# Performance work log

Hardware: AMD Instinct MI355X
Metric: run time of the kernel (lower is better)

Reference implementation:

```python
import jax, jax.numpy as jnp
import numpy as np
from jax import lax

EMB_DIM = 16
NUM_EMB = 32
DN = ('NCDHW', 'OIDHW', 'NCDHW')


def conv3d(x, w, b, stride, pad):
    y = lax.conv_general_dilated(x, w, window_strides=(stride,) * 3,
                                 padding=[(pad, pad)] * 3, dimension_numbers=DN)
    return y + b[None, :, None, None, None]


def deconv3d(x, w, b, stride, pad):
    # PyTorch ConvTranspose3d: weight (Cin,Cout,k,k,k); equivalent to conv with
    # spatially flipped, channel-transposed kernel, lhs_dilation=stride, pad=k-1-p.
    k = w.shape[-1]
    wf = jnp.flip(w, axis=(2, 3, 4)).transpose(1, 0, 2, 3, 4)  # (Cout,Cin,k,k,k)
    y = lax.conv_general_dilated(x, wf, window_strides=(1, 1, 1),
                                 padding=[(k - 1 - pad, k - 1 - pad)] * 3,
                                 lhs_dilation=(stride,) * 3, dimension_numbers=DN)
    return y + b[None, :, None, None, None]


def setup_inputs() -> dict:
    key = jax.random.key(0)
    ks = jax.random.split(key, 16)
    x = jax.random.normal(ks[0], (16, 3, 16, 128, 128), dtype=jnp.float32)
    s = 0.05
    # encoder params
    enc_w1 = jax.random.normal(ks[1], (4, 3, 4, 4, 4), jnp.float32) * s
    enc_b1 = jnp.zeros((4,), jnp.float32)
    enc_w2 = jax.random.normal(ks[2], (8, 4, 4, 4, 4), jnp.float32) * s
    enc_b2 = jnp.zeros((8,), jnp.float32)
    enc_w4 = jax.random.normal(ks[3], (EMB_DIM, 8, 3, 3, 3), jnp.float32) * s
    enc_b4 = jnp.zeros((EMB_DIM,), jnp.float32)
    # decoder params (ConvTranspose3d layout: (Cin, Cout, k, k, k))
    dec_w1 = jax.random.normal(ks[4], (EMB_DIM, 8, 4, 4, 4), jnp.float32) * s
    dec_b1 = jnp.zeros((8,), jnp.float32)
    dec_w3 = jax.random.normal(ks[5], (8, 4, 4, 4, 4), jnp.float32) * s
    dec_b3 = jnp.zeros((4,), jnp.float32)
    dec_w4 = jax.random.normal(ks[6], (4, 3, 3, 3, 3), jnp.float32) * s
    dec_b4 = jnp.zeros((3,), jnp.float32)
    # codebook buffers: normalize(randn)*0.1, rows 0/1 forced
    e = jax.random.normal(ks[7], (NUM_EMB, EMB_DIM), jnp.float32)
    e = e / jnp.linalg.norm(e, axis=1, keepdims=True) * 0.1
    embedding = e.at[0].set(0.0).at[1].set(6.0)
    cluster_size = jnp.ones((NUM_EMB,), jnp.float32)
    return dict(x=x, epoch=60,
                enc_w1=enc_w1, enc_b1=enc_b1, enc_w2=enc_w2, enc_b2=enc_b2,
                enc_w4=enc_w4, enc_b4=enc_b4,
                dec_w1=dec_w1, dec_b1=dec_b1, dec_w3=dec_w3, dec_b3=dec_b3,
                dec_w4=dec_w4, dec_b4=dec_b4,
                embedding=embedding, cluster_size=cluster_size)


def reference(x, epoch, enc_w1, enc_b1, enc_w2, enc_b2, enc_w4, enc_b4,
              dec_w1, dec_b1, dec_w3, dec_b3, dec_w4, dec_b4,
              embedding, cluster_size):
    # ---- Encoder ----
    h = jax.nn.relu(conv3d(x, enc_w1, enc_b1, 2, 1))
    h = jax.nn.relu(conv3d(h, enc_w2, enc_b2, 2, 1))
    z = jnp.clip(conv3d(h, enc_w4, enc_b4, 1, 1), 0.0, 6.0)  # relu(relu6(.))
    B, C, Dd, Hh, Ww = z.shape

    # ---- VQ-EMA forward (epoch >= 50 branch) ----
    emb = embedding.at[0].set(0.0).at[1].set(6.0)
    flat = z.transpose(0, 2, 3, 4, 1).reshape(-1, C)  # (N, D)
    # squared euclidean distances; argmin matches cdist argmin
    d2 = (jnp.sum(flat * flat, axis=1, keepdims=True)
          - 2.0 * flat @ emb.T + jnp.sum(emb * emb, axis=1))
    idx = jnp.argmin(d2, axis=1)                       # (N,)
    q = emb[idx]                                       # (N, D)
    quant = q.reshape(B, Dd, Hh, Ww, C).transpose(0, 4, 1, 2, 3)

    N = flat.shape[0]
    avg_probs = jnp.zeros((NUM_EMB,), flat.dtype).at[idx].add(1.0) / N
    perplexity = jnp.exp(-jnp.sum(avg_probs * jnp.log(avg_probs + 1e-10)))
    used_codes = jnp.sum(cluster_size > 1e-5).astype(jnp.float32) / NUM_EMB

    quantized_st = z + lax.stop_gradient(quant - z)
    vq_loss = 0.25 * jnp.mean((lax.stop_gradient(quant) - z) ** 2)
    codes = idx.reshape(B, Dd, Hh, Ww)

    # ---- Decoder ----
    d = jax.nn.relu(deconv3d(quantized_st, dec_w1, dec_b1, 2, 1))
    d = jax.nn.relu(deconv3d(d, dec_w3, dec_b3, 2, 1))
    out = deconv3d(d, dec_w4, dec_b4, 1, 1)
    return out, vq_loss, codes, perplexity, used_codes
```

## Files before the change

kernel.cpp:

```cpp
#include <hip/hip_runtime.h>
#include <math.h>

#define NB 16


#define P_STRIDE 136
#define P_PLANE  (130 * P_STRIDE)
#define P_VOL    (18 * P_PLANE)
#define D1_STRIDE 72
#define D1_PLANE  (66 * D1_STRIDE)
#define D1_VOL    (10 * D1_PLANE)

__device__ __forceinline__ float4 ld4(const float* p) {
  return *reinterpret_cast<const float4*>(p);
}
__device__ __forceinline__ void st4(float* p, float4 v) {
  *reinterpret_cast<float4*>(p) = v;
}

__global__ __launch_bounds__(256) void conv1_k(
    const float* __restrict__ x, const float* __restrict__ w,
    const float* __restrict__ bias, float* __restrict__ y) {
  int idx = blockIdx.x * 256 + threadIdx.x;
  int g  = idx & 15;
  int oh = (idx >> 4) & 63;
  int od = (idx >> 10) & 7;
  int n  = idx >> 13;
  bool gl = (g > 0), gr = (g < 15);
  float acc[4][4];
  #pragma unroll
  for (int co = 0; co < 4; co++) {
    float bv = bias[co];
    #pragma unroll
    for (int m = 0; m < 4; m++) acc[co][m] = bv;
  }
  int ih0 = 2 * oh - 1;
  #pragma unroll 1
  for (int ci = 0; ci < 3; ci++) {
    #pragma unroll 1
    for (int kd = 0; kd < 4; kd++) {
      int id = 2 * od - 1 + kd;
      bool vd = (unsigned)id < 16u;
      int idc = vd ? id : 0;
      const float* plane = x + (((n * 3 + ci) * 16 + idc) * 16384);
      #pragma unroll
      for (int kh = 0; kh < 4; kh++) {
        int ih = ih0 + kh;
        bool v = vd && ((unsigned)ih < 128u);
        int ihc = (unsigned)ih < 128u ? ih : 0;
        const float* rp = plane + ihc * 128 + 8 * g;
        float r[10];
        float4 A = ld4(rp);
        float4 B = ld4(rp + 4);
        float rl = rp[-1 * (int)gl];
        float rr = rp[gr ? 8 : 0];
        r[0] = (v && gl) ? rl : 0.0f;
        r[1] = v ? A.x : 0.0f; r[2] = v ? A.y : 0.0f;
        r[3] = v ? A.z : 0.0f; r[4] = v ? A.w : 0.0f;
        r[5] = v ? B.x : 0.0f; r[6] = v ? B.y : 0.0f;
        r[7] = v ? B.z : 0.0f; r[8] = v ? B.w : 0.0f;
        r[9] = (v && gr) ? rr : 0.0f;
        #pragma unroll
        for (int co = 0; co < 4; co++) {
          const float* wb = w + ((co * 3 + ci) * 4 + kd) * 16 + kh * 4;
          #pragma unroll
          for (int kw = 0; kw < 4; kw++) {
            float wv = wb[kw];
            #pragma unroll
            for (int m = 0; m < 4; m++)
              acc[co][m] += r[2 * m + kw] * wv;
          }
        }
      }
    }
  }
  #pragma unroll
  for (int co = 0; co < 4; co++) {
    float4 o;
    o.x = fmaxf(acc[co][0], 0.0f); o.y = fmaxf(acc[co][1], 0.0f);
    o.z = fmaxf(acc[co][2], 0.0f); o.w = fmaxf(acc[co][3], 0.0f);
    st4(y + ((n * 4 + co) * 8 + od) * 4096 + oh * 64 + 4 * g, o);
  }
}

__global__ __launch_bounds__(256) void conv2_k(
    const float* __restrict__ y1, const float* __restrict__ w,
    const float* __restrict__ bias, float* __restrict__ y) {
  int idx = blockIdx.x * 256 + threadIdx.x;
  int ow = idx & 31;
  int oh = (idx >> 5) & 31;
  int od = (idx >> 10) & 3;
  int n = (idx >> 12) & 15;
  int cog = idx >> 16;
  float acc[4];
  #pragma unroll
  for (int co = 0; co < 4; co++) acc[co] = bias[cog * 4 + co];
  int id0 = 2 * od - 1, ih0 = 2 * oh - 1, iw0 = 2 * ow - 1;
  bool vh[4], vw[4];
  #pragma unroll
  for (int l = 0; l < 4; l++) {
    vh[l] = (unsigned)(ih0 + l) < 64u;
    vw[l] = (unsigned)(iw0 + l) < 64u;
  }
  #pragma unroll 1
  for (int ci = 0; ci < 4; ci++) {
    const float* ip = y1 + ((n * 4 + ci) * 8) * 4096;
    #pragma unroll
    for (int kd = 0; kd < 4; kd++) {
      int id = id0 + kd;
      bool vd = (unsigned)id < 8u;
      const float* pp = ip + id * 4096;
      float p[4][4];
      #pragma unroll
      for (int kh = 0; kh < 4; kh++)
        #pragma unroll
        for (int kw = 0; kw < 4; kw++)
          p[kh][kw] = (vd && vh[kh] && vw[kw]) ? pp[(ih0 + kh) * 64 + (iw0 + kw)] : 0.0f;
      #pragma unroll
      for (int co = 0; co < 4; co++) {
        const float* wp = w + (((cog * 4 + co) * 4 + ci) * 4 + kd) * 16;
        #pragma unroll
        for (int kh = 0; kh < 4; kh++)
          #pragma unroll
          for (int kw = 0; kw < 4; kw++)
            acc[co] += p[kh][kw] * wp[kh * 4 + kw];
      }
    }
  }
  #pragma unroll
  for (int co = 0; co < 4; co++)
    y[((n * 8 + cog * 4 + co) * 4 + od) * 1024 + oh * 32 + ow] = fmaxf(acc[co], 0.0f);
}

__global__ __launch_bounds__(256) void conv4_k(
    const float* __restrict__ y2, const float* __restrict__ w,
    const float* __restrict__ bias, float* __restrict__ z) {
  int idx = blockIdx.x * 256 + threadIdx.x;
  int ow = idx & 31;
  int oh = (idx >> 5) & 31;
  int od = (idx >> 10) & 3;
  int n = (idx >> 12) & 15;
  int cog = idx >> 16;
  float acc[4];
  #pragma unroll
  for (int co = 0; co < 4; co++) acc[co] = bias[cog * 4 + co];
  bool vh[3], vw[3];
  #pragma unroll
  for (int l = 0; l < 3; l++) {
    vh[l] = (unsigned)(oh - 1 + l) < 32u;
    vw[l] = (unsigned)(ow - 1 + l) < 32u;
  }
  #pragma unroll 1
  for (int ci = 0; ci < 8; ci++) {
    const float* ip = y2 + ((n * 8 + ci) * 4) * 1024;
    #pragma unroll
    for (int kd = 0; kd < 3; kd++) {
      int id = od - 1 + kd;
      bool vd = (unsigned)id < 4u;
      const float* pp = ip + id * 1024;
      float p[3][3];
      #pragma unroll
      for (int kh = 0; kh < 3; kh++)
        #pragma unroll
        for (int kw = 0; kw < 3; kw++)
          p[kh][kw] = (vd && vh[kh] && vw[kw]) ? pp[(oh - 1 + kh) * 32 + (ow - 1 + kw)] : 0.0f;
      #pragma unroll
      for (int co = 0; co < 4; co++) {
        const float* wp = w + (((cog * 4 + co) * 8 + ci) * 3 + kd) * 9;
        #pragma unroll
        for (int kh = 0; kh < 3; kh++)
          #pragma unroll
          for (int kw = 0; kw < 3; kw++)
            acc[co] += p[kh][kw] * wp[kh * 3 + kw];
      }
    }
  }
  #pragma unroll
  for (int co = 0; co < 4; co++)
    z[((n * 16 + cog * 4 + co) * 4 + od) * 1024 + oh * 32 + ow] =
        fminf(fmaxf(acc[co], 0.0f), 6.0f);
}

__global__ __launch_bounds__(256) void vq_k(
    const float* __restrict__ z, const float* __restrict__ emb,
    float* __restrict__ quant, float* __restrict__ codes_out,
    float* __restrict__ stats) {
  __shared__ float se[32 * 16];
  __shared__ float se2[32];
  __shared__ float shist[32];
  __shared__ float swred[4];
  int tid = threadIdx.x;
  for (int i = tid; i < 512; i += 256) {
    int r = i >> 4;
    float v = emb[i];
    if (r == 0) v = 0.0f;
    else if (r == 1) v = 6.0f;
    se[i] = v;
  }
  if (tid < 32) shist[tid] = 0.0f;
  __syncthreads();
  if (tid < 32) {
    float s = 0.0f;
    #pragma unroll
    for (int d = 0; d < 16; d++) { float v = se[tid * 16 + d]; s += v * v; }
    se2[tid] = s;
  }
  __syncthreads();

  int idx = blockIdx.x * 256 + tid;
  float lsum = 0.0f;
  {
    int w_ = idx & 31; int t = idx >> 5;
    int h_ = t & 31; t >>= 5;
    int d_ = t & 3;  int b_ = t >> 2;
    const float* zp = z + b_ * 65536 + d_ * 1024 + h_ * 32 + w_;
    float f[16];
    float f2 = 0.0f;
    #pragma unroll
    for (int c = 0; c < 16; c++) { float v = zp[c * 4096]; f[c] = v; f2 += v * v; }
    float best = 1e30f; int bi = 0;
    for (int e = 0; e < 32; e++) {
      float dot = 0.0f;
      #pragma unroll
      for (int c = 0; c < 16; c++) dot += f[c] * se[e * 16 + c];
      float d2 = f2 - 2.0f * dot + se2[e];
      if (d2 < best) { best = d2; bi = e; }
    }
    float* qp = quant + b_ * 65536 + d_ * 1024 + h_ * 32 + w_;
    #pragma unroll
    for (int c = 0; c < 16; c++) {
      float q = se[bi * 16 + c];
      qp[c * 4096] = q;
      float df = q - f[c];
      lsum += df * df;
    }
    codes_out[idx] = (float)bi;
    atomicAdd(&shist[bi], 1.0f);
  }
  for (int o = 32; o; o >>= 1) lsum += __shfl_down(lsum, o);
  if ((tid & 63) == 0) swred[tid >> 6] = lsum;
  __syncthreads();
  if (tid == 0) atomicAdd(&stats[0], swred[0] + swred[1] + swred[2] + swred[3]);
  if (tid < 32) {
    float h = shist[tid];
    if (h != 0.0f) atomicAdd(&stats[1 + tid], h);
  }
}

__global__ void init_stats_k(float* __restrict__ stats) {
  int tid = threadIdx.x;
  if (tid < 33) stats[tid] = 0.0f;
}

__global__ void fin_k(const float* __restrict__ stats,
                      const float* __restrict__ cluster_size,
                      float* __restrict__ out_loss, float* __restrict__ out_perp,
                      float* __restrict__ out_used) {
  int tid = threadIdx.x;
  float v = 0.0f;
  float used = 0.0f;
  if (tid < 32) {
    float p = stats[1 + tid] * (1.0f / 65536.0f);
    v = p * logf(p + 1e-10f);
    used = (cluster_size[tid] > 1e-5f) ? 1.0f : 0.0f;
  }
  for (int o = 16; o; o >>= 1) { v += __shfl_down(v, o); used += __shfl_down(used, o); }
  if (tid == 0) {
    *out_perp = expf(-v);
    *out_used = used * (1.0f / 32.0f);
    *out_loss = 0.25f * stats[0] * (1.0f / 1048576.0f);
  }
}

template <int PADDED>
__global__ __launch_bounds__(256) void deconv1_t(
    const float* __restrict__ q, const float* __restrict__ w,
    const float* __restrict__ bias, float* __restrict__ d1) {
  int bid = blockIdx.x;
  int cog = bid & 1;
  int ph  = (bid >> 1) & 1;
  int od  = (bid >> 2) & 7;
  int n   = bid >> 5;
  int tid = threadIdx.x;
  int g   = tid & 7;
  int bl  = tid >> 3;
  bool glf = (g > 0), grf = (g < 7);

  int kd0 = (od + 1) & 1;
  int idtop = (od + 1 - kd0) >> 1;
  int kh0 = (ph + 1) & 1;
  int ihtop = bl + ph;

  float acc[4][8];
  #pragma unroll
  for (int co = 0; co < 4; co++) {
    float bv = bias[cog * 4 + co];
    #pragma unroll
    for (int m = 0; m < 8; m++) acc[co][m] = bv;
  }

  #pragma unroll 1
  for (int ci = 0; ci < 16; ci++) {
    const float* ip = q + ((n * 16 + ci) * 4) * 1024;
    #pragma unroll
    for (int jd = 0; jd < 2; jd++) {
      int id = idtop - jd;
      bool vd = (unsigned)id < 4u;
      int idc = vd ? id : 0;
      const float* plane = ip + idc * 1024;
      #pragma unroll
      for (int jh = 0; jh < 2; jh++) {
        int ih = ihtop - jh;
        bool v = vd && ((unsigned)ih < 32u);
        int ihc = (unsigned)ih < 32u ? ih : 0;
        const float* rp = plane + ihc * 32 + 4 * g;
        float r[6];
        float4 A = ld4(rp);
        float rl = rp[-1 * (int)glf];
        float rr = rp[grf ? 4 : 0];
        r[0] = (v && glf) ? rl : 0.0f;
        r[1] = v ? A.x : 0.0f; r[2] = v ? A.y : 0.0f;
        r[3] = v ? A.z : 0.0f; r[4] = v ? A.w : 0.0f;
        r[5] = (v && grf) ? rr : 0.0f;
        int kd = kd0 + 2 * jd;
        int kh = kh0 + 2 * jh;
        #pragma unroll
        for (int co = 0; co < 4; co++) {
          const float* wb = w + ((ci * 8 + cog * 4 + co) * 4 + kd) * 16 + kh * 4;
          #pragma unroll
          for (int jw = 0; jw < 2; jw++) {
            float w_ev = wb[1 + 2 * jw];
            float w_od = wb[2 * jw];
            #pragma unroll
            for (int ii = 0; ii < 4; ii++) {
              acc[co][2 * ii]     += r[ii + 1 - jw] * w_ev;
              acc[co][2 * ii + 1] += r[ii + 2 - jw] * w_od;
            }
          }
        }
      }
    }
  }
  int oh = 2 * bl + ph;
  #pragma unroll
  for (int co = 0; co < 4; co++) {
    float* op;
    if (PADDED)
      op = d1 + (size_t)(n * 8 + cog * 4 + co) * D1_VOL +
           (od + 1) * D1_PLANE + (oh + 1) * D1_STRIDE + 8 * g + 4;
    else
      op = d1 + ((n * 8 + cog * 4 + co) * 8 + od) * 4096 + oh * 64 + 8 * g;
    float4 lo, hi;
    lo.x = fmaxf(acc[co][0], 0.0f); lo.y = fmaxf(acc[co][1], 0.0f);
    lo.z = fmaxf(acc[co][2], 0.0f); lo.w = fmaxf(acc[co][3], 0.0f);
    hi.x = fmaxf(acc[co][4], 0.0f); hi.y = fmaxf(acc[co][5], 0.0f);
    hi.z = fmaxf(acc[co][6], 0.0f); hi.w = fmaxf(acc[co][7], 0.0f);
    st4(op, lo); st4(op + 4, hi);
  }
}

template <int INP, int OUTP>
__global__ __launch_bounds__(256) void deconv3_t(
    const float* __restrict__ d1, const float* __restrict__ w,
    const float* __restrict__ bias, float* __restrict__ d2) {
  int bid = blockIdx.x;
  int ph  = bid & 1;
  int blh = (bid >> 1) & 3;
  int od  = (bid >> 3) & 15;
  int n   = bid >> 7;
  int tid = threadIdx.x;
  int g   = tid & 15;
  int bl  = tid >> 4;
  int BL  = blh * 16 + bl;
  bool glf = (g > 0), grf = (g < 15);

  int kd0 = (od + 1) & 1;
  int idtop = (od + 1 - kd0) >> 1;
  int kh0 = (ph + 1) & 1;
  int ihtop = BL + ph;

  float acc[4][8];
  #pragma unroll
  for (int co = 0; co < 4; co++) {
    float bv = bias[co];
    #pragma unroll
    for (int m = 0; m < 8; m++) acc[co][m] = bv;
  }

  #pragma unroll 1
  for (int ci = 0; ci < 8; ci++) {
    #pragma unroll
    for (int jd = 0; jd < 2; jd++) {
      #pragma unroll
      for (int jh = 0; jh < 2; jh++) {
        float r[6];
        if (INP) {
          const float* rp = d1 + (size_t)(n * 8 + ci) * D1_VOL +
                            (idtop + 1 - jd) * D1_PLANE + (ihtop + 1 - jh) * D1_STRIDE +
                            4 * g + 4;
          float4 A = ld4(rp);
          r[0] = rp[-1];
          r[1] = A.x; r[2] = A.y; r[3] = A.z; r[4] = A.w;
          r[5] = rp[4];
        } else {
          const float* ip = d1 + ((n * 8 + ci) * 8) * 4096;
          int id = idtop - jd;
          bool vd = (unsigned)id < 8u;
          int idc = vd ? id : 0;
          const float* plane = ip + idc * 4096;
          int ih = ihtop - jh;
          bool v = vd && ((unsigned)ih < 64u);
          int ihc = (unsigned)ih < 64u ? ih : 0;
          const float* rp = plane + ihc * 64 + 4 * g;
          float4 A = ld4(rp);
          float rl = rp[-1 * (int)glf];
          float rr = rp[grf ? 4 : 0];
          r[0] = (v && glf) ? rl : 0.0f;
          r[1] = v ? A.x : 0.0f; r[2] = v ? A.y : 0.0f;
          r[3] = v ? A.z : 0.0f; r[4] = v ? A.w : 0.0f;
          r[5] = (v && grf) ? rr : 0.0f;
        }
        int kd = kd0 + 2 * jd;
        int kh = kh0 + 2 * jh;
        #pragma unroll
        for (int co = 0; co < 4; co++) {
          const float* wb = w + ((ci * 4 + co) * 4 + kd) * 16 + kh * 4;
          #pragma unroll
          for (int jw = 0; jw < 2; jw++) {
            float w_ev = wb[1 + 2 * jw];
            float w_od = wb[2 * jw];
            #pragma unroll
            for (int ii = 0; ii < 4; ii++) {
              acc[co][2 * ii]     += r[ii + 1 - jw] * w_ev;
              acc[co][2 * ii + 1] += r[ii + 2 - jw] * w_od;
            }
          }
        }
      }
    }
  }
  int oh = 2 * BL + ph;
  #pragma unroll
  for (int co = 0; co < 4; co++) {
    float* op;
    if (OUTP)
      op = d2 + (size_t)(n * 4 + co) * P_VOL + (od + 1) * P_PLANE + (oh + 1) * P_STRIDE + 8 * g + 4;
    else
      op = d2 + ((n * 4 + co) * 16 + od) * 16384 + oh * 128 + 8 * g;
    float4 lo, hi;
    lo.x = fmaxf(acc[co][0], 0.0f); lo.y = fmaxf(acc[co][1], 0.0f);
    lo.z = fmaxf(acc[co][2], 0.0f); lo.w = fmaxf(acc[co][3], 0.0f);
    hi.x = fmaxf(acc[co][4], 0.0f); hi.y = fmaxf(acc[co][5], 0.0f);
    hi.z = fmaxf(acc[co][6], 0.0f); hi.w = fmaxf(acc[co][7], 0.0f);
    st4(op, lo); st4(op + 4, hi);
  }
}

__global__ __launch_bounds__(256) void zero_halo_k(float* __restrict__ d2p) {
  const int PER = 43808;
  int total = PER * 64;
  for (int i = blockIdx.x * 256 + threadIdx.x; i < total; i += gridDim.x * 256) {
    int nc = i / PER;
    int j = i - nc * PER;
    int elem;
    if (j < 35360) {
      int pd = (j < 17680) ? 0 : 17;
      int off = (j < 17680) ? j : j - 17680;
      elem = pd * P_PLANE + off;
    } else if (j < 39712) {
      int k = j - 35360;
      int pd = 1 + (k / 272);
      int rj = k - (pd - 1) * 272;
      int row = (rj < 136) ? 0 : 129;
      int col = (rj < 136) ? rj : rj - 136;
      elem = pd * P_PLANE + row * P_STRIDE + col;
    } else {
      int k = j - 39712;
      int pd = 1 + (k / 256);
      int rj = k - (pd - 1) * 256;
      int row = 1 + (rj >> 1);
      int col = (rj & 1) ? 132 : 3;
      elem = pd * P_PLANE + row * P_STRIDE + col;
    }
    d2p[(size_t)nc * P_VOL + elem] = 0.0f;
  }
}

__global__ __launch_bounds__(256) void zero_halo_d1p_k(float* __restrict__ d1p) {
  const int PER = 11680;
  int total = PER * 128;
  for (int i = blockIdx.x * 256 + threadIdx.x; i < total; i += gridDim.x * 256) {
    int nc = i / PER;
    int j = i - nc * PER;
    int elem;
    if (j < 9504) {
      int pd = (j < 4752) ? 0 : 9;
      int off = (j < 4752) ? j : j - 4752;
      elem = pd * D1_PLANE + off;
    } else if (j < 10656) {
      int k = j - 9504;
      int pd = 1 + (k / 144);
      int rj = k - (pd - 1) * 144;
      int row = (rj < 72) ? 0 : 65;
      int col = (rj < 72) ? rj : rj - 72;
      elem = pd * D1_PLANE + row * D1_STRIDE + col;
    } else {
      int k = j - 10656;
      int pd = 1 + (k / 128);
      int rj = k - (pd - 1) * 128;
      int row = 1 + (rj >> 1);
      int col = (rj & 1) ? 68 : 3;
      elem = pd * D1_PLANE + row * D1_STRIDE + col;
    }
    d1p[(size_t)nc * D1_VOL + elem] = 0.0f;
  }
}

__global__ __launch_bounds__(256) void deconv4_k(
    const float* __restrict__ d2, const float* __restrict__ w,
    const float* __restrict__ bias, float* __restrict__ out) {
  int idx = blockIdx.x * 256 + threadIdx.x;
  int c = idx & 63;
  int b = (idx >> 6) & 63;
  int a = (idx >> 12) & 7;
  int n = idx >> 15;
  float acc[2][2][2][3];
  #pragma unroll
  for (int pd = 0; pd < 2; pd++)
    #pragma unroll
    for (int ph = 0; ph < 2; ph++)
      #pragma unroll
      for (int pw = 0; pw < 2; pw++)
        #pragma unroll
        for (int co = 0; co < 3; co++) acc[pd][ph][pw][co] = bias[co];
  int ih0 = 2 * b - 1, iw0 = 2 * c - 1;
  bool vh[4], vw[4];
  #pragma unroll
  for (int l = 0; l < 4; l++) {
    vh[l] = (unsigned)(ih0 + l) < 128u;
    vw[l] = (unsigned)(iw0 + l) < 128u;
  }
  #pragma unroll 1
  for (int ci = 0; ci < 4; ci++) {
    const float* ip = d2 + ((n * 4 + ci) * 16) * 16384;
    #pragma unroll
    for (int ld = 0; ld < 4; ld++) {
      int id = 2 * a - 1 + ld;
      bool vdl = (unsigned)id < 16u;
      const float* pp = ip + id * 16384;
      float p[4][4];
      #pragma unroll
      for (int lh = 0; lh < 4; lh++)
        #pragma unroll
        for (int lw = 0; lw < 4; lw++)
          p[lh][lw] = (vdl && vh[lh] && vw[lw]) ? pp[(ih0 + lh) * 128 + (iw0 + lw)] : 0.0f;
      #pragma unroll
      for (int pd = 0; pd < 2; pd++) {
        int kd = pd + 2 - ld;
        if (kd < 0 || kd > 2) continue;
        #pragma unroll
        for (int kh = 0; kh < 3; kh++)
          #pragma unroll
          for (int kw = 0; kw < 3; kw++)
            #pragma unroll
            for (int co = 0; co < 3; co++) {
              float wv = w[(ci * 3 + co) * 27 + kd * 9 + kh * 3 + kw];
              #pragma unroll
              for (int ph = 0; ph < 2; ph++)
                #pragma unroll
                for (int pw = 0; pw < 2; pw++)
                  acc[pd][ph][pw][co] += p[ph + 2 - kh][pw + 2 - kw] * wv;
            }
      }
    }
  }
  #pragma unroll
  for (int co = 0; co < 3; co++)
    #pragma unroll
    for (int pd = 0; pd < 2; pd++)
      #pragma unroll
      for (int ph = 0; ph < 2; ph++)
        #pragma unroll
        for (int pw = 0; pw < 2; pw++)
          out[((n * 3 + co) * 16 + 2 * a + pd) * 16384 +
              (2 * b + ph) * 128 + (2 * c + pw)] = acc[pd][ph][pw][co];
}

__global__ __launch_bounds__(256) void deconv4p_k(
    const float* __restrict__ d2p, const float* __restrict__ w,
    const float* __restrict__ bias, float* __restrict__ out) {
  int idx = blockIdx.x * 256 + threadIdx.x;
  int c = idx & 31;
  int b = (idx >> 5) & 63;
  int a = (idx >> 11) & 7;
  int n = idx >> 14;
  float acc[2][2][3][4];
  #pragma unroll
  for (int pd = 0; pd < 2; pd++)
    #pragma unroll
    for (int ph = 0; ph < 2; ph++)
      #pragma unroll
      for (int co = 0; co < 3; co++) {
        float bv = bias[co];
        #pragma unroll
        for (int pw = 0; pw < 4; pw++) acc[pd][ph][co][pw] = bv;
      }
  #pragma unroll 1
  for (int ci = 0; ci < 4; ci++) {
    const float* ip = d2p + (size_t)(n * 4 + ci) * P_VOL +
                      (2 * a) * P_PLANE + (2 * b) * P_STRIDE + (4 * c);
    #pragma unroll
    for (int ld = 0; ld < 4; ld++) {
      const float* pp = ip + ld * P_PLANE;
      float pr[4][12];
      #pragma unroll
      for (int lh = 0; lh < 4; lh++) {
        const float* rp = pp + lh * P_STRIDE;
        float4 A = ld4(rp);
        float4 B = ld4(rp + 4);
        float4 C = ld4(rp + 8);
        pr[lh][0] = A.x;  pr[lh][1] = A.y;  pr[lh][2] = A.z;  pr[lh][3] = A.w;
        pr[lh][4] = B.x;  pr[lh][5] = B.y;  pr[lh][6] = B.z;  pr[lh][7] = B.w;
        pr[lh][8] = C.x;  pr[lh][9] = C.y;  pr[lh][10] = C.z; pr[lh][11] = C.w;
      }
      #pragma unroll
      for (int pd = 0; pd < 2; pd++) {
        int kd = pd + 2 - ld;
        if (kd < 0 || kd > 2) continue;
        #pragma unroll
        for (int kh = 0; kh < 3; kh++)
          #pragma unroll
          for (int kw = 0; kw < 3; kw++)
            #pragma unroll
            for (int co = 0; co < 3; co++) {
              float wv = w[(ci * 3 + co) * 27 + kd * 9 + kh * 3 + kw];
              #pragma unroll
              for (int ph = 0; ph < 2; ph++)
                #pragma unroll
                for (int pw = 0; pw < 4; pw++)
                  acc[pd][ph][co][pw] += pr[ph + 2 - kh][pw + 5 - kw] * wv;
            }
      }
    }
  }
  #pragma unroll
  for (int co = 0; co < 3; co++)
    #pragma unroll
    for (int pd = 0; pd < 2; pd++)
      #pragma unroll
      for (int ph = 0; ph < 2; ph++) {
        float4 o;
        o.x = acc[pd][ph][co][0]; o.y = acc[pd][ph][co][1];
        o.z = acc[pd][ph][co][2]; o.w = acc[pd][ph][co][3];
        st4(out + ((n * 3 + co) * 16 + 2 * a + pd) * 16384 +
            (2 * b + ph) * 128 + 4 * c, o);
      }
}

extern "C" void kernel_launch(void* const* d_in, const int* in_sizes, int n_in,
                              void* d_out, int out_size, void* d_ws, size_t ws_size,
                              hipStream_t stream) {
  const float* x      = (const float*)d_in[0];
  const float* enc_w1 = (const float*)d_in[2];
  const float* enc_b1 = (const float*)d_in[3];
  const float* enc_w2 = (const float*)d_in[4];
  const float* enc_b2 = (const float*)d_in[5];
  const float* enc_w4 = (const float*)d_in[6];
  const float* enc_b4 = (const float*)d_in[7];
  const float* dec_w1 = (const float*)d_in[8];
  const float* dec_b1 = (const float*)d_in[9];
  const float* dec_w3 = (const float*)d_in[10];
  const float* dec_b3 = (const float*)d_in[11];
  const float* dec_w4 = (const float*)d_in[12];
  const float* dec_b4 = (const float*)d_in[13];
  const float* emb    = (const float*)d_in[14];
  const float* csize  = (const float*)d_in[15];

  float* ws = (float*)d_ws;
  float* stats = ws;
  float* quant = ws + 64;
  float* z     = quant + 1048576;
  float* y2    = z + 1048576;
  float* y1    = y2 + 524288;

  float* out   = (float*)d_out;
  float* out_loss  = out + 12582912;
  float* out_codes = out_loss + 1;
  float* out_perp  = out_codes + 65536;
  float* out_used  = out_perp + 1;

  const size_t FULL_NEED = (size_t)(64 + 1048576 + 6082560 + 20367360) * sizeof(float);
  const size_t MID_NEED  = (size_t)(64 + 1048576 + 4194304 + 20367360) * sizeof(float);

  init_stats_k<<<1, 64, 0, stream>>>(stats);

  conv1_k<<<512, 256, 0, stream>>>(x, enc_w1, enc_b1, y1);
  conv2_k<<<512, 256, 0, stream>>>(y1, enc_w2, enc_b2, y2);
  conv4_k<<<1024, 256, 0, stream>>>(y2, enc_w4, enc_b4, z);

  vq_k<<<256, 256, 0, stream>>>(z, emb, quant, out_codes, stats);
  fin_k<<<1, 64, 0, stream>>>(stats, csize, out_loss, out_perp, out_used);

  if (ws_size >= FULL_NEED) {
    float* d1p = ws + 64 + 1048576;
    float* d2p = d1p + 6082560;
    zero_halo_k<<<1024, 256, 0, stream>>>(d2p);
    zero_halo_d1p_k<<<1024, 256, 0, stream>>>(d1p);
    deconv1_t<1><<<512, 256, 0, stream>>>(quant, dec_w1, dec_b1, d1p);
    deconv3_t<1, 1><<<2048, 256, 0, stream>>>(d1p, dec_w3, dec_b3, d2p);
    deconv4p_k<<<1024, 256, 0, stream>>>(d2p, dec_w4, dec_b4, out);
  } else if (ws_size >= MID_NEED) {
    float* d1  = ws + 64 + 1048576;
    float* d2p = d1 + 4194304;
    zero_halo_k<<<1024, 256, 0, stream>>>(d2p);
    deconv1_t<0><<<512, 256, 0, stream>>>(quant, dec_w1, dec_b1, d1);
    deconv3_t<0, 1><<<2048, 256, 0, stream>>>(d1, dec_w3, dec_b3, d2p);
    deconv4p_k<<<1024, 256, 0, stream>>>(d2p, dec_w4, dec_b4, out);
  } else {
    float* d1 = ws + 64 + 1048576;
    float* d2 = d1 + 4194304;
    deconv1_t<0><<<512, 256, 0, stream>>>(quant, dec_w1, dec_b1, d1);
    deconv3_t<0, 0><<<2048, 256, 0, stream>>>(d1, dec_w3, dec_b3, d2);
    deconv4_k<<<2048, 256, 0, stream>>>(d2, dec_w4, dec_b4, out);
  }
}
```

Measured before the change: 349.0 us.

## Widen deconv3 per-thread output tile and trim deconv4 padded-row loads

Adds a new deconv3 kernel in which each thread computes 16 contiguous output columns for 4 channels. It uses the parity decomposition of the stride-2 transposed conv, so each loaded input row of 10 values feeds both even and odd outputs, and it runs on half as many blocks. Separately, the deconv4 padded kernel now loads only the 6 needed values per row (one float4 plus two scalars) instead of three float4s. The aim is fewer redundant global loads and more reuse per thread, at the cost of more accumulator registers and possibly lower occupancy.

```diff
diff --git a/kernel.cpp b/kernel.cpp
--- a/kernel.cpp
+++ b/kernel.cpp
@@ -456,6 +456,84 @@
   }
 }
 
+__global__ __launch_bounds__(256) void deconv3w_k(
+    const float* __restrict__ d1p, const float* __restrict__ w,
+    const float* __restrict__ bias, float* __restrict__ d2p) {
+  int bid = blockIdx.x;
+  int ph  = bid & 1;
+  int blh = (bid >> 1) & 1;
+  int od  = (bid >> 2) & 15;
+  int n   = bid >> 6;
+  int tid = threadIdx.x;
+  int g   = tid & 7;
+  int bl  = tid >> 3;
+  int BL  = blh * 32 + bl;
+
+  int kd0 = (od + 1) & 1;
+  int idtop = (od + 1 - kd0) >> 1;
+  int kh0 = (ph + 1) & 1;
+  int ihtop = BL + ph;
+
+  float acc[4][16];
+  #pragma unroll
+  for (int co = 0; co < 4; co++) {
+    float bv = bias[co];
+    #pragma unroll
+    for (int m = 0; m < 16; m++) acc[co][m] = bv;
+  }
+
+  #pragma unroll 1
+  for (int ci = 0; ci < 8; ci++) {
+    #pragma unroll
+    for (int jd = 0; jd < 2; jd++) {
+      #pragma unroll
+      for (int jh = 0; jh < 2; jh++) {
+        const float* rp = d1p + (size_t)(n * 8 + ci) * D1_VOL +
+                          (idtop + 1 - jd) * D1_PLANE + (ihtop + 1 - jh) * D1_STRIDE +
+                          8 * g + 4;
+        float r[10];
+        float4 A = ld4(rp);
+        float4 B = ld4(rp + 4);
+        r[0] = rp[-1];
+        r[1] = A.x; r[2] = A.y; r[3] = A.z; r[4] = A.w;
+        r[5] = B.x; r[6] = B.y; r[7] = B.z; r[8] = B.w;
+        r[9] = rp[8];
+        int kd = kd0 + 2 * jd;
+        int kh = kh0 + 2 * jh;
+        #pragma unroll
+        for (int co = 0; co < 4; co++) {
+          const float* wb = w + ((ci * 4 + co) * 4 + kd) * 16 + kh * 4;
+          #pragma unroll
+          for (int jw = 0; jw < 2; jw++) {
+            float w_ev = wb[1 + 2 * jw];
+            float w_od = wb[2 * jw];
+            #pragma unroll
+            for (int ii = 0; ii < 8; ii++) {
+              acc[co][2 * ii]     += r[ii + 1 - jw] * w_ev;
+              acc[co][2 * ii + 1] += r[ii + 2 - jw] * w_od;
+            }
+          }
+        }
+      }
+    }
+  }
+  int oh = 2 * BL + ph;
+  #pragma unroll
+  for (int co = 0; co < 4; co++) {
+    float* op = d2p + (size_t)(n * 4 + co) * P_VOL +
+                (od + 1) * P_PLANE + (oh + 1) * P_STRIDE + 16 * g + 4;
+    #pragma unroll
+    for (int qd = 0; qd < 4; qd++) {
+      float4 o;
+      o.x = fmaxf(acc[co][4 * qd], 0.0f);
+      o.y = fmaxf(acc[co][4 * qd + 1], 0.0f);
+      o.z = fmaxf(acc[co][4 * qd + 2], 0.0f);
+      o.w = fmaxf(acc[co][4 * qd + 3], 0.0f);
+      st4(op + 4 * qd, o);
+    }
+  }
+}
+
 __global__ __launch_bounds__(256) void zero_halo_k(float* __restrict__ d2p) {
   const int PER = 43808;
   int total = PER * 64;
@@ -612,16 +690,14 @@
     #pragma unroll
     for (int ld = 0; ld < 4; ld++) {
       const float* pp = ip + ld * P_PLANE;
-      float pr[4][12];
+      float rr[4][6];
       #pragma unroll
       for (int lh = 0; lh < 4; lh++) {
         const float* rp = pp + lh * P_STRIDE;
-        float4 A = ld4(rp);
-        float4 B = ld4(rp + 4);
-        float4 C = ld4(rp + 8);
-        pr[lh][0] = A.x;  pr[lh][1] = A.y;  pr[lh][2] = A.z;  pr[lh][3] = A.w;
-        pr[lh][4] = B.x;  pr[lh][5] = B.y;  pr[lh][6] = B.z;  pr[lh][7] = B.w;
-        pr[lh][8] = C.x;  pr[lh][9] = C.y;  pr[lh][10] = C.z; pr[lh][11] = C.w;
+        float4 A = ld4(rp + 4);
+        rr[lh][0] = rp[3];
+        rr[lh][1] = A.x; rr[lh][2] = A.y; rr[lh][3] = A.z; rr[lh][4] = A.w;
+        rr[lh][5] = rp[8];
       }
       #pragma unroll
       for (int pd = 0; pd < 2; pd++) {
@@ -638,7 +714,7 @@
               for (int ph = 0; ph < 2; ph++)
                 #pragma unroll
                 for (int pw = 0; pw < 4; pw++)
-                  acc[pd][ph][co][pw] += pr[ph + 2 - kh][pw + 5 - kw] * wv;
+                  acc[pd][ph][co][pw] += rr[ph + 2 - kh][pw + 2 - kw] * wv;
             }
       }
     }
@@ -707,7 +783,7 @@
     zero_halo_k<<<1024, 256, 0, stream>>>(d2p);
     zero_halo_d1p_k<<<1024, 256, 0, stream>>>(d1p);
     deconv1_t<1><<<512, 256, 0, stream>>>(quant, dec_w1, dec_b1, d1p);
-    deconv3_t<1, 1><<<2048, 256, 0, stream>>>(d1p, dec_w3, dec_b3, d2p);
+    deconv3w_k<<<1024, 256, 0, stream>>>(d1p, dec_w3, dec_b3, d2p);
     deconv4p_k<<<1024, 256, 0, stream>>>(d2p, dec_w4, dec_b4, out);
   } else if (ws_size >= MID_NEED) {
     float* d1  = ws + 64 + 1048576;
```

Measured after the change: 357.7 us. 2.5% more time.
